# Performance work log

Hardware: AMD Instinct MI355X
Metric: run time of the kernel (lower is better)

The kernel has to match this reference:

```python
import jax, jax.numpy as jnp
import numpy as np

N = 512   # particles
T = 128   # timesteps
V_L = 3.4
V_0 = 4.2
GAMMA = 0.9
ALPHA = 0.15
BETA = 15.0
E_CRIT_INV = 2e-5
F_STD = 0.05
G_STD = 0.02
NU = 1.0 / (G_STD * float(np.sqrt(2.0 * np.pi)))
CUR_MIN = 0.0
CUR_MAX = 1.0


def voc(soc):
    # open-circuit voltage model
    return (V_L + (V_0 - V_L) * jnp.exp(GAMMA * (soc - 1.0))
            + ALPHA * V_L * (soc - 1.0)
            + (1.0 - ALPHA) * V_L * (jnp.exp(-BETA) - jnp.exp(-BETA * jnp.sqrt(soc))))


def mlp(x, w1, b1, w2, b2, w3, b3):
    h = jax.nn.sigmoid(x @ w1 + b1)
    h = jax.nn.sigmoid(h @ w2 + b2)
    return h @ w3 + b3


def setup_inputs() -> dict:
    key = jax.random.key(0)
    ks = jax.random.split(key, 11)
    soc_init = jax.random.uniform(ks[0], (N, 1), jnp.float32, 0.6, 1.0)
    current = jax.random.uniform(ks[1], (1, T), jnp.float32)
    voltage_measured = 3.4 + 0.8 * jax.random.uniform(ks[2], (1, T), jnp.float32)
    noise = jax.random.normal(ks[3], (T, N, 1), jnp.float32)
    u = jax.random.uniform(ks[4], (T,), jnp.float32)
    w1 = jax.random.normal(ks[5], (2, 1024), jnp.float32) / np.float32(np.sqrt(2.0))
    b1 = jnp.zeros((1024,), jnp.float32)
    w2 = jax.random.normal(ks[6], (1024, 512), jnp.float32) / np.float32(np.sqrt(1024.0))
    b2 = jnp.zeros((512,), jnp.float32)
    w3 = jax.random.normal(ks[7], (512, 1), jnp.float32) / np.float32(np.sqrt(512.0))
    b3 = jnp.zeros((1,), jnp.float32)
    return {"soc_init": soc_init, "current": current, "voltage_measured": voltage_measured,
            "noise": noise, "u": u, "w1": w1, "b1": b1, "w2": w2, "b2": b2, "w3": w3, "b3": b3}


def reference(soc_init, current, voltage_measured, noise, u, w1, b1, w2, b2, w3, b3):
    n = soc_init.shape[0]
    # pre-loop step: V at t=0 conditions
    I0 = current[0, 0] * jnp.ones_like(soc_init)
    sI0 = (I0 - CUR_MIN) / (CUR_MAX - CUR_MIN)
    Z0 = mlp(jnp.concatenate([soc_init, sI0], axis=1), w1, b1, w2, b2, w3, b3)
    V0 = voc(soc_init) - I0 * Z0

    log_n = jnp.log(jnp.float32(n))

    def step(carry, xs):
        soc, I, V = carry
        cur_t, vmeas_t, noise_t, u_t = xs
        # state propagation with process noise, then clamp to (0, 1]
        soc = soc - I * V * E_CRIT_INV + F_STD * noise_t
        soc = jnp.where(soc > 1.0, 1.0, jnp.where(soc < 0.0, 1e-10, soc))
        I = cur_t * jnp.ones_like(soc)
        sI = (I - CUR_MIN) / (CUR_MAX - CUR_MIN)
        Z = mlp(jnp.concatenate([soc, sI], axis=1), w1, b1, w2, b2, w3, b3)  # [N,1]
        V = voc(soc) - I * Z                                                 # [N,1]
        # importance weights / step loss (logsumexp trick as in source)
        logW = jnp.log(jnp.float32(NU)) - 0.5 * jnp.square((V - vmeas_t) / G_STD)
        step_loss = jax.nn.logsumexp(logW) - log_n
        # systematic resampling on normalized weights
        wn = jax.nn.softmax(logW[:, 0])          # normalized weights [N]
        cum = jnp.cumsum(wn)
        pos = (jnp.arange(n, dtype=jnp.float32) + u_t) / jnp.float32(n)
        idx = jnp.clip(jnp.searchsorted(cum, pos), 0, n - 1)
        soc_r = soc[idx]
        return (soc_r, I, V), (V[:, 0], soc_r[:, 0], step_loss)

    xs = (current[0], voltage_measured[0], noise, u)
    _, (v_hist, s_hist, losses) = jax.lax.scan(step, (soc_init, I0, V0), xs)
    loss = jnp.sum(losses)
    voltage = v_hist.T    # [N, T]
    soc_hist = s_hist.T   # [N, T]
    return loss, voltage, soc_hist
```

## Files before the change

kernel.cpp:

```cpp
#include <hip/hip_runtime.h>
#include <hip/hip_bf16.h>
#include <math.h>

#define N_PART 512
#define T_STEPS 128
#define G_NODES 33
#define TAB2D (G_NODES * G_NODES)
#define ROWS (T_STEPS * G_NODES)
#define V_L 3.4f
#define V_0 4.2f
#define GAMMA 0.9f
#define ALPHA 0.15f
#define BETA 15.0f
#define E_CRIT_INV 2e-5f
#define F_STD 0.05f
#define G_STD 0.02f

#define LBAR() asm volatile("s_waitcnt lgkmcnt(0)\n\ts_barrier" ::: "memory")

__device__ __forceinline__ float sigmoid_jax(float x) {
    float e = expf(-fabsf(x));
    float num = (x >= 0.f) ? 1.f : e;
    return num / (1.f + e);
}

__device__ __forceinline__ float vocf(float s) {
    float sm1 = s - 1.f;
    return V_L + (V_0 - V_L) * expf(GAMMA * sm1)
         + (ALPHA * V_L) * sm1
         + (1.f - ALPHA) * V_L * (expf(-BETA) - expf(-BETA * sqrtf(s)));
}

template <int R>
__device__ __forceinline__ int dpp_ror(int v) {
    return __builtin_amdgcn_update_dpp(0, v, 0x120 | R, 0xf, 0xf, false);
}
template <int S>
__device__ __forceinline__ int dpp_shr(int v) {
    return __builtin_amdgcn_update_dpp(0, v, 0x110 | S, 0xf, 0xf, true);
}
__device__ __forceinline__ float fror(float v, float o) { return o; }

__device__ __forceinline__ float wave_max_f(float v) {
    v = fmaxf(v, __int_as_float(dpp_ror<1>(__float_as_int(v))));
    v = fmaxf(v, __int_as_float(dpp_ror<2>(__float_as_int(v))));
    v = fmaxf(v, __int_as_float(dpp_ror<4>(__float_as_int(v))));
    v = fmaxf(v, __int_as_float(dpp_ror<8>(__float_as_int(v))));
    int iv = __float_as_int(v);
    v = fmaxf(v, __int_as_float(__builtin_amdgcn_update_dpp(iv, iv, 0x142, 0xf, 0xf, false)));
    iv = __float_as_int(v);
    v = fmaxf(v, __int_as_float(__builtin_amdgcn_update_dpp(iv, iv, 0x143, 0xf, 0xf, false)));
    return __int_as_float(__builtin_amdgcn_readlane(__float_as_int(v), 63));
}

__device__ __forceinline__ int wave_max_i(int v) {
    v = max(v, dpp_ror<1>(v));
    v = max(v, dpp_ror<2>(v));
    v = max(v, dpp_ror<4>(v));
    v = max(v, dpp_ror<8>(v));
    v = max(v, __builtin_amdgcn_update_dpp(v, v, 0x142, 0xf, 0xf, false));
    v = max(v, __builtin_amdgcn_update_dpp(v, v, 0x143, 0xf, 0xf, false));
    return __builtin_amdgcn_readlane(v, 63);
}

__device__ __forceinline__ float wave_scan_add(float v, int lane) {
    v += __int_as_float(dpp_shr<1>(__float_as_int(v)));
    v += __int_as_float(dpp_shr<2>(__float_as_int(v)));
    v += __int_as_float(dpp_shr<4>(__float_as_int(v)));
    v += __int_as_float(dpp_shr<8>(__float_as_int(v)));
    float s15 = __int_as_float(__builtin_amdgcn_readlane(__float_as_int(v), 15));
    float s31 = __int_as_float(__builtin_amdgcn_readlane(__float_as_int(v), 31));
    float s47 = __int_as_float(__builtin_amdgcn_readlane(__float_as_int(v), 47));
    int row = lane >> 4;
    if (row >= 1) v += s15;
    if (row >= 2) v += s31;
    if (row >= 3) v += s47;
    return v;
}

__device__ __forceinline__ int wave_scanmax_i(int v, int lane) {
    v = max(v, dpp_shr<1>(v));
    v = max(v, dpp_shr<2>(v));
    v = max(v, dpp_shr<4>(v));
    v = max(v, dpp_shr<8>(v));
    int r15 = __builtin_amdgcn_readlane(v, 15);
    int r31 = __builtin_amdgcn_readlane(v, 31);
    int r47 = __builtin_amdgcn_readlane(v, 47);
    int row = lane >> 4;
    if (row >= 1) v = max(v, r15);
    if (row >= 2) v = max(v, r31);
    if (row >= 3) v = max(v, r47);
    return v;
}

#define BKT 32
__global__ __launch_bounds__(256) void k_tab(
    const float* __restrict__ w1, const float* __restrict__ b1,
    const float* __restrict__ w2, const float* __restrict__ b2,
    const float* __restrict__ w3, float* __restrict__ zpart)
{
    const int tid = threadIdx.x;
    const int rowblk = blockIdx.x >> 1;
    const int colhalf = blockIdx.x & 1;
    const int r0 = rowblk * 8;
    const int cbase = colhalf * 256;

    __shared__ float As[8][BKT + 1];
    __shared__ float Bs[BKT][256];
    __shared__ float srow[8], irow[8];

    if (tid < 8) {
        int r = r0 + tid;
        r = r > (TAB2D - 1) ? (TAB2D - 1) : r;
        int si = r / G_NODES;
        int ii = r - si * G_NODES;
        srow[tid] = (float)si * (1.0f / 32.0f);
        irow[tid] = (float)ii * (1.0f / 32.0f);
    }
    __syncthreads();

    const int rg = tid >> 5;
    const int ct = tid & 31;
    float acc[8];
    #pragma unroll
    for (int b = 0; b < 8; ++b) acc[b] = 0.f;

    for (int kk = 0; kk < 1024; kk += BKT) {
        {
            int kc = kk + ct;
            float pre = srow[rg] * w1[kc] + irow[rg] * w1[1024 + kc] + b1[kc];
            As[rg][ct] = sigmoid_jax(pre);
        }
        #pragma unroll
        for (int jj = 0; jj < 8; ++jj) {
            int vi = tid + jj * 256;
            int k = vi >> 6, c4 = vi & 63;
            *(float4*)&Bs[k][c4 * 4] = *(const float4*)&w2[(kk + k) * 512 + cbase + c4 * 4];
        }
        __syncthreads();
        #pragma unroll
        for (int k = 0; k < BKT; ++k) {
            float a = As[rg][k];
            float bq[8];
            *(float4*)&bq[0] = *(const float4*)&Bs[k][ct * 4];
            *(float4*)&bq[4] = *(const float4*)&Bs[k][ct * 4 + 128];
            #pragma unroll
            for (int q = 0; q < 8; ++q) acc[q] += a * bq[q];
        }
        __syncthreads();
    }

    float b2r[8], w3r[8];
    *(float4*)&b2r[0] = *(const float4*)&b2[cbase + ct * 4];
    *(float4*)&b2r[4] = *(const float4*)&b2[cbase + ct * 4 + 128];
    *(float4*)&w3r[0] = *(const float4*)&w3[cbase + ct * 4];
    *(float4*)&w3r[4] = *(const float4*)&w3[cbase + ct * 4 + 128];
    float zp = 0.f;
    #pragma unroll
    for (int q = 0; q < 8; ++q)
        zp += w3r[q] * sigmoid_jax(acc[q] + b2r[q]);
    #pragma unroll
    for (int mm = 1; mm < 32; mm <<= 1) zp += __shfl_xor(zp, mm);
    if (ct == 0 && (r0 + rg) < TAB2D)
        zpart[colhalf * TAB2D + r0 + rg] = zp;
}

__device__ __forceinline__ float interp_tab(const float* __restrict__ row, int stride, float s) {
    float x = s * 32.0f;
    int j = (int)floorf(x);
    j = j < 0 ? 0 : (j > 31 ? 31 : j);
    int st = j - 1;
    st = st < 0 ? 0 : (st > 29 ? 29 : st);
    float uu = x - (float)st;
    float um0 = uu, um1 = uu - 1.f, um2 = uu - 2.f, um3 = uu - 3.f;
    float w0 = um1 * um2 * um3 * (-1.f / 6.f);
    float w1 = um0 * um2 * um3 * (0.5f);
    float w2 = um0 * um1 * um3 * (-0.5f);
    float w3 = um0 * um1 * um2 * (1.f / 6.f);
    return w0 * row[st * stride] + w1 * row[(st + 1) * stride]
         + w2 * row[(st + 2) * stride] + w3 * row[(st + 3) * stride];
}

__device__ __forceinline__ int count_le(float C, float u) {
    int h = (int)floorf(C - u);
    h = h < -1 ? -1 : (h > 511 ? 511 : h);
    h += (int)((h < 511) && (((float)(h + 1) + u) <= C));
    h += (int)((h < 511) && (((float)(h + 1) + u) <= C));
    h -= (int)((h >= 0) && (((float)h + u) > C));
    h -= (int)((h >= 0) && (((float)h + u) > C));
    return h + 1;
}

__global__ __launch_bounds__(512, 1) void k_seq(
    const float* __restrict__ zpart, const float* __restrict__ soc_init,
    const float* __restrict__ current, const float* __restrict__ vmeas,
    const float* __restrict__ u, const float* __restrict__ noise,
    const float* __restrict__ b3, float* __restrict__ vbuf,
    float* __restrict__ sbuf, float* __restrict__ out)
{
    const int tid = threadIdx.x;
    const int lane = tid & 63;
    const int wid = tid >> 6;

    __shared__ float zt[ROWS];
    __shared__ float zt2d[TAB2D];
    __shared__ float socs[2][512];
    __shared__ int marker[512];
    __shared__ float cur_s[128], vm_s[128], u_s[128];
    __shared__ float redM[8], redT[8];

    float bb3 = b3[0];
    for (int j = tid; j < TAB2D; j += 512) zt2d[j] = zpart[j] + zpart[TAB2D + j] + bb3;
    if (tid < 128) { cur_s[tid] = current[tid]; vm_s[tid] = vmeas[tid]; u_s[tid] = u[tid]; }
    marker[tid] = 0;
    __syncthreads();

    for (int idx = tid; idx < ROWS; idx += 512) {
        int t = idx / G_NODES;
        int g = idx - t * G_NODES;
        zt[idx] = interp_tab(&zt2d[g * G_NODES], 1, cur_s[t]);
    }
    __syncthreads();

    float soc = soc_init[tid];
    float Iprev = cur_s[0];
    float V = vocf(soc) - Iprev * interp_tab(&zt[0], 1, soc);
    float loss_acc = 0.f;
    const float LOG_NU = logf(19.947114020071635f);
    const float LOG_N = logf(512.f);

    float nz_cur = noise[tid];

    for (int t = 0; t < T_STEPS; ++t) {
        int tn = (t + 1 < T_STEPS) ? t + 1 : t;
        float nz_next = noise[tn * 512 + tid];

        soc = soc - Iprev * V * E_CRIT_INV + F_STD * nz_cur;
        soc = soc > 1.f ? 1.f : (soc < 0.f ? 1e-10f : soc);
        socs[t & 1][tid] = soc;

        float I = cur_s[t];
        V = vocf(soc) - I * interp_tab(&zt[t * G_NODES], 1, soc);
        float d = (V - vm_s[t]) * (1.f / G_STD);
        float lw = LOG_NU - 0.5f * d * d;

        float m = wave_max_f(lw);
        float e = expf(lw - m);
        float incl = wave_scan_add(e, lane);
        if (lane == 63) { redM[wid] = m; redT[wid] = incl; }
        LBAR();

        float rm = redM[lane & 7];
        float rt = redT[lane & 7];
        float M = rm;
        M = fmaxf(M, __int_as_float(dpp_ror<1>(__float_as_int(M))));
        M = fmaxf(M, __int_as_float(dpp_ror<2>(__float_as_int(M))));
        M = fmaxf(M, __int_as_float(dpp_ror<4>(__float_as_int(M))));
        M = fmaxf(M, __int_as_float(dpp_ror<8>(__float_as_int(M))));
        float fw = expf(rm - M);
        float term = rt * fw;
        float sc = term;
        sc += __int_as_float(dpp_shr<1>(__float_as_int(sc)));
        sc += __int_as_float(dpp_shr<2>(__float_as_int(sc)));
        sc += __int_as_float(dpp_shr<4>(__float_as_int(sc)));
        float S = __int_as_float(__builtin_amdgcn_readlane(__float_as_int(sc), 7));
        float off = 0.f;
        if (wid > 0) off = __int_as_float(__builtin_amdgcn_readlane(__float_as_int(sc), wid - 1));
        float fw_own = __int_as_float(__builtin_amdgcn_readlane(__float_as_int(fw), wid));
        loss_acc += M + logf(S) - LOG_N;

        float C = 512.f * ((off + incl * fw_own) / S);
        int hi = count_le(C, u_s[t]);
        if (hi < 512) atomicMax(&marker[hi], (t << 10) | (tid + 1));
        LBAR();

        int pm = 0;
        for (int w = 0; w < wid; ++w) pm = max(pm, marker[w * 64 + lane]);
        pm = wave_max_i(pm);
        int v = wave_scanmax_i(marker[tid], lane);
        int sv = max(v, pm);
        int owner = ((sv >> 10) == t) ? (sv & 1023) : 0;
        owner = owner > 511 ? 511 : owner;
        float socr = socs[t & 1][owner];

        vbuf[t * 512 + tid] = V;
        sbuf[t * 512 + tid] = socr;
        soc = socr;
        Iprev = I;
        nz_cur = nz_next;
    }
    if (tid == 0) out[0] = loss_acc;
}

__global__ __launch_bounds__(256) void k_fin(
    const float* __restrict__ vbuf, const float* __restrict__ sbuf,
    float* __restrict__ out)
{
    __shared__ float tile[32][33];
    int tz = blockIdx.z;
    int t0 = blockIdx.x * 32;
    int i0 = blockIdx.y * 32;
    const float* src = tz ? sbuf : vbuf;
    float* dst = out + 1 + tz * (N_PART * T_STEPS);
    int tx = threadIdx.x & 31, ty = threadIdx.x >> 5;
    #pragma unroll
    for (int m2 = 0; m2 < 4; ++m2)
        tile[ty + 8 * m2][tx] = src[(t0 + ty + 8 * m2) * 512 + i0 + tx];
    __syncthreads();
    #pragma unroll
    for (int m2 = 0; m2 < 4; ++m2)
        dst[(i0 + ty + 8 * m2) * 128 + t0 + tx] = tile[tx][ty + 8 * m2];
}

extern "C" void kernel_launch(void* const* d_in, const int* in_sizes, int n_in,
                              void* d_out, int out_size, void* d_ws, size_t ws_size,
                              hipStream_t stream)
{
    const float* soc_init = (const float*)d_in[0];
    const float* current  = (const float*)d_in[1];
    const float* vmeas    = (const float*)d_in[2];
    const float* noise    = (const float*)d_in[3];
    const float* u        = (const float*)d_in[4];
    const float* w1 = (const float*)d_in[5];
    const float* b1 = (const float*)d_in[6];
    const float* w2 = (const float*)d_in[7];
    const float* b2 = (const float*)d_in[8];
    const float* w3 = (const float*)d_in[9];
    const float* b3 = (const float*)d_in[10];
    float* out = (float*)d_out;
    float* ws  = (float*)d_ws;

    float* zpart = ws;
    float* vbuf  = ws + 2 * TAB2D;
    float* sbuf  = vbuf + N_PART * T_STEPS;

    k_tab<<<274, 256, 0, stream>>>(w1, b1, w2, b2, w3, zpart);
    k_seq<<<1, 512, 0, stream>>>(zpart, soc_init, current, vmeas, u, noise, b3,
                                 vbuf, sbuf, out);
    k_fin<<<dim3(4, 16, 2), 256, 0, stream>>>(vbuf, sbuf, out);
}
```

Baseline: 286.2 us.

## Replace marker-based resampling with direct range scatter and retile table GEMM

The resampling step now has each particle compute its lower and upper cumulative-count bounds and write its SOC into the resampled slots it owns. This replaces the atomicMax marker array and the prefix-max scans that followed it. The cross-wave combine now uses readlane broadcasts instead of DPP scans, and exp/log switch to the fast intrinsics. The table-building kernel handles 16 rows per block with one column per thread, halving the block count. These changes shorten the serial per-timestep critical path, at the cost of a per-thread loop that can be uneven and slightly lower-precision exp/log.

```diff
diff --git a/kernel.cpp b/kernel.cpp
--- a/kernel.cpp
+++ b/kernel.cpp
@@ -1,20 +1,19 @@
 #include <hip/hip_runtime.h>
-#include <hip/hip_bf16.h>
 #include <math.h>
 
-#define N_PART 512
-#define T_STEPS 128
-#define G_NODES 33
-#define TAB2D (G_NODES * G_NODES)
-#define ROWS (T_STEPS * G_NODES)
-#define V_L 3.4f
-#define V_0 4.2f
-#define GAMMA 0.9f
-#define ALPHA 0.15f
-#define BETA 15.0f
-#define E_CRIT_INV 2e-5f
-#define F_STD 0.05f
-#define G_STD 0.02f
+#define NP 512
+#define TS 128
+#define GI 33
+#define TAB2D (GI * GI)
+#define ROWS (TS * GI)
+#define V_Lc 3.4f
+#define V_0c 4.2f
+#define GAMMAc 0.9f
+#define ALPHAc 0.15f
+#define BETAc 15.0f
+#define E_INV 2e-5f
+#define F_STDc 0.05f
+#define G_STDc 0.02f
 
 #define LBAR() asm volatile("s_waitcnt lgkmcnt(0)\n\ts_barrier" ::: "memory")
 
@@ -26,9 +25,9 @@
 
 __device__ __forceinline__ float vocf(float s) {
     float sm1 = s - 1.f;
-    return V_L + (V_0 - V_L) * expf(GAMMA * sm1)
-         + (ALPHA * V_L) * sm1
-         + (1.f - ALPHA) * V_L * (expf(-BETA) - expf(-BETA * sqrtf(s)));
+    return V_Lc + (V_0c - V_Lc) * expf(GAMMAc * sm1)
+         + (ALPHAc * V_Lc) * sm1
+         + (1.f - ALPHAc) * V_Lc * (expf(-BETAc) - expf(-BETAc * sqrtf(s)));
 }
 
 template <int R>
@@ -39,7 +38,9 @@
 __device__ __forceinline__ int dpp_shr(int v) {
     return __builtin_amdgcn_update_dpp(0, v, 0x110 | S, 0xf, 0xf, true);
 }
-__device__ __forceinline__ float fror(float v, float o) { return o; }
+__device__ __forceinline__ float rdlane_f(float v, int l) {
+    return __int_as_float(__builtin_amdgcn_readlane(__float_as_int(v), l));
+}
 
 __device__ __forceinline__ float wave_max_f(float v) {
     v = fmaxf(v, __int_as_float(dpp_ror<1>(__float_as_int(v))));
@@ -50,17 +51,7 @@
     v = fmaxf(v, __int_as_float(__builtin_amdgcn_update_dpp(iv, iv, 0x142, 0xf, 0xf, false)));
     iv = __float_as_int(v);
     v = fmaxf(v, __int_as_float(__builtin_amdgcn_update_dpp(iv, iv, 0x143, 0xf, 0xf, false)));
-    return __int_as_float(__builtin_amdgcn_readlane(__float_as_int(v), 63));
-}
-
-__device__ __forceinline__ int wave_max_i(int v) {
-    v = max(v, dpp_ror<1>(v));
-    v = max(v, dpp_ror<2>(v));
-    v = max(v, dpp_ror<4>(v));
-    v = max(v, dpp_ror<8>(v));
-    v = max(v, __builtin_amdgcn_update_dpp(v, v, 0x142, 0xf, 0xf, false));
-    v = max(v, __builtin_amdgcn_update_dpp(v, v, 0x143, 0xf, 0xf, false));
-    return __builtin_amdgcn_readlane(v, 63);
+    return rdlane_f(v, 63);
 }
 
 __device__ __forceinline__ float wave_scan_add(float v, int lane) {
@@ -68,9 +59,9 @@
     v += __int_as_float(dpp_shr<2>(__float_as_int(v)));
     v += __int_as_float(dpp_shr<4>(__float_as_int(v)));
     v += __int_as_float(dpp_shr<8>(__float_as_int(v)));
-    float s15 = __int_as_float(__builtin_amdgcn_readlane(__float_as_int(v), 15));
-    float s31 = __int_as_float(__builtin_amdgcn_readlane(__float_as_int(v), 31));
-    float s47 = __int_as_float(__builtin_amdgcn_readlane(__float_as_int(v), 47));
+    float s15 = rdlane_f(v, 15);
+    float s31 = rdlane_f(v, 31);
+    float s47 = rdlane_f(v, 47);
     int row = lane >> 4;
     if (row >= 1) v += s15;
     if (row >= 2) v += s31;
@@ -78,58 +69,80 @@
     return v;
 }
 
-__device__ __forceinline__ int wave_scanmax_i(int v, int lane) {
-    v = max(v, dpp_shr<1>(v));
-    v = max(v, dpp_shr<2>(v));
-    v = max(v, dpp_shr<4>(v));
-    v = max(v, dpp_shr<8>(v));
-    int r15 = __builtin_amdgcn_readlane(v, 15);
-    int r31 = __builtin_amdgcn_readlane(v, 31);
-    int r47 = __builtin_amdgcn_readlane(v, 47);
-    int row = lane >> 4;
-    if (row >= 1) v = max(v, r15);
-    if (row >= 2) v = max(v, r31);
-    if (row >= 3) v = max(v, r47);
-    return v;
-}
-
-#define BKT 32
+__device__ __forceinline__ float shfl_up1_f(float v, int lane, float lane0val) {
+    float pv = __int_as_float(dpp_shr<1>(__float_as_int(v)));
+    float r15 = rdlane_f(v, 15);
+    float r31 = rdlane_f(v, 31);
+    float r47 = rdlane_f(v, 47);
+    if (lane == 16) pv = r15;
+    if (lane == 32) pv = r31;
+    if (lane == 48) pv = r47;
+    if (lane == 0)  pv = lane0val;
+    return pv;
+}
+
+__device__ __forceinline__ float interp_z(const float* __restrict__ row, float s) {
+    float x = s * 32.0f;
+    int j = (int)floorf(x);
+    j = j < 0 ? 0 : (j > 31 ? 31 : j);
+    int st = j - 1;
+    st = st < 0 ? 0 : (st > 29 ? 29 : st);
+    float uu = x - (float)st;
+    float um0 = uu, um1 = uu - 1.f, um2 = uu - 2.f, um3 = uu - 3.f;
+    float c0 = um1 * um2 * um3 * (-1.f / 6.f);
+    float c1 = um0 * um2 * um3 * (0.5f);
+    float c2 = um0 * um1 * um3 * (-0.5f);
+    float c3 = um0 * um1 * um2 * (1.f / 6.f);
+    return c0 * row[st] + c1 * row[st + 1] + c2 * row[st + 2] + c3 * row[st + 3];
+}
+
+__device__ __forceinline__ int count_le(float C, float u) {
+    int h = (int)floorf(C - u);
+    h = h < -1 ? -1 : (h > 511 ? 511 : h);
+    h += (int)((h < 511) && (((float)(h + 1) + u) <= C));
+    h += (int)((h < 511) && (((float)(h + 1) + u) <= C));
+    h -= (int)((h >= 0) && (((float)h + u) > C));
+    h -= (int)((h >= 0) && (((float)h + u) > C));
+    return h + 1;
+}
+
 __global__ __launch_bounds__(256) void k_tab(
     const float* __restrict__ w1, const float* __restrict__ b1,
     const float* __restrict__ w2, const float* __restrict__ b2,
     const float* __restrict__ w3, float* __restrict__ zpart)
 {
     const int tid = threadIdx.x;
+    const int lane = tid & 63;
+    const int wv = tid >> 6;
     const int rowblk = blockIdx.x >> 1;
     const int colhalf = blockIdx.x & 1;
-    const int r0 = rowblk * 8;
+    const int r0 = rowblk * 16;
     const int cbase = colhalf * 256;
 
-    __shared__ float As[8][BKT + 1];
-    __shared__ float Bs[BKT][256];
-    __shared__ float srow[8], irow[8];
-
-    if (tid < 8) {
-        int r = r0 + tid;
-        r = r > (TAB2D - 1) ? (TAB2D - 1) : r;
-        int si = r / G_NODES;
-        int ii = r - si * G_NODES;
+    __shared__ float As[16][33];
+    __shared__ float Bs[32][256];
+    __shared__ float srow[16], irow[16];
+    __shared__ float red[16][4];
+
+    if (tid < 16) {
+        int r = r0 + tid; if (r > TAB2D - 1) r = TAB2D - 1;
+        int si = r / GI, ii = r - si * GI;
         srow[tid] = (float)si * (1.0f / 32.0f);
         irow[tid] = (float)ii * (1.0f / 32.0f);
     }
     __syncthreads();
 
-    const int rg = tid >> 5;
-    const int ct = tid & 31;
-    float acc[8];
+    float acc[16];
     #pragma unroll
-    for (int b = 0; b < 8; ++b) acc[b] = 0.f;
-
-    for (int kk = 0; kk < 1024; kk += BKT) {
-        {
-            int kc = kk + ct;
-            float pre = srow[rg] * w1[kc] + irow[rg] * w1[1024 + kc] + b1[kc];
-            As[rg][ct] = sigmoid_jax(pre);
+    for (int r = 0; r < 16; ++r) acc[r] = 0.f;
+
+    for (int kk = 0; kk < 1024; kk += 32) {
+        #pragma unroll
+        for (int h = 0; h < 2; ++h) {
+            int idx = tid + h * 256;
+            int row = idx >> 5, k = idx & 31, kc = kk + k;
+            float pre = srow[row] * w1[kc] + irow[row] * w1[1024 + kc] + b1[kc];
+            As[row][k] = sigmoid_jax(pre);
         }
         #pragma unroll
         for (int jj = 0; jj < 8; ++jj) {
@@ -139,56 +152,28 @@
         }
         __syncthreads();
         #pragma unroll
-        for (int k = 0; k < BKT; ++k) {
-            float a = As[rg][k];
-            float bq[8];
-            *(float4*)&bq[0] = *(const float4*)&Bs[k][ct * 4];
-            *(float4*)&bq[4] = *(const float4*)&Bs[k][ct * 4 + 128];
+        for (int k = 0; k < 32; ++k) {
+            float bv = Bs[k][tid];
             #pragma unroll
-            for (int q = 0; q < 8; ++q) acc[q] += a * bq[q];
+            for (int r = 0; r < 16; ++r) acc[r] += As[r][k] * bv;
         }
         __syncthreads();
     }
 
-    float b2r[8], w3r[8];
-    *(float4*)&b2r[0] = *(const float4*)&b2[cbase + ct * 4];
-    *(float4*)&b2r[4] = *(const float4*)&b2[cbase + ct * 4 + 128];
-    *(float4*)&w3r[0] = *(const float4*)&w3[cbase + ct * 4];
-    *(float4*)&w3r[4] = *(const float4*)&w3[cbase + ct * 4 + 128];
-    float zp = 0.f;
+    float b2c = b2[cbase + tid];
+    float w3c = w3[cbase + tid];
     #pragma unroll
-    for (int q = 0; q < 8; ++q)
-        zp += w3r[q] * sigmoid_jax(acc[q] + b2r[q]);
-    #pragma unroll
-    for (int mm = 1; mm < 32; mm <<= 1) zp += __shfl_xor(zp, mm);
-    if (ct == 0 && (r0 + rg) < TAB2D)
-        zpart[colhalf * TAB2D + r0 + rg] = zp;
-}
-
-__device__ __forceinline__ float interp_tab(const float* __restrict__ row, int stride, float s) {
-    float x = s * 32.0f;
-    int j = (int)floorf(x);
-    j = j < 0 ? 0 : (j > 31 ? 31 : j);
-    int st = j - 1;
-    st = st < 0 ? 0 : (st > 29 ? 29 : st);
-    float uu = x - (float)st;
-    float um0 = uu, um1 = uu - 1.f, um2 = uu - 2.f, um3 = uu - 3.f;
-    float w0 = um1 * um2 * um3 * (-1.f / 6.f);
-    float w1 = um0 * um2 * um3 * (0.5f);
-    float w2 = um0 * um1 * um3 * (-0.5f);
-    float w3 = um0 * um1 * um2 * (1.f / 6.f);
-    return w0 * row[st * stride] + w1 * row[(st + 1) * stride]
-         + w2 * row[(st + 2) * stride] + w3 * row[(st + 3) * stride];
-}
-
-__device__ __forceinline__ int count_le(float C, float u) {
-    int h = (int)floorf(C - u);
-    h = h < -1 ? -1 : (h > 511 ? 511 : h);
-    h += (int)((h < 511) && (((float)(h + 1) + u) <= C));
-    h += (int)((h < 511) && (((float)(h + 1) + u) <= C));
-    h -= (int)((h >= 0) && (((float)h + u) > C));
-    h -= (int)((h >= 0) && (((float)h + u) > C));
-    return h + 1;
+    for (int r = 0; r < 16; ++r) {
+        float zp = w3c * sigmoid_jax(acc[r] + b2c);
+        #pragma unroll
+        for (int mm = 1; mm < 64; mm <<= 1) zp += __shfl_xor(zp, mm);
+        if (lane == 0) red[r][wv] = zp;
+    }
+    __syncthreads();
+    if (tid < 16 && (r0 + tid) < TAB2D) {
+        float s = ((red[tid][0] + red[tid][1]) + red[tid][2]) + red[tid][3];
+        zpart[colhalf * TAB2D + r0 + tid] = s;
+    }
 }
 
 __global__ __launch_bounds__(512, 1) void k_seq(
@@ -200,90 +185,81 @@
 {
     const int tid = threadIdx.x;
     const int lane = tid & 63;
-    const int wid = tid >> 6;
-
-    __shared__ float zt[ROWS];
+    const int wv = tid >> 6;
+    const int swv = __builtin_amdgcn_readfirstlane(wv);
+
+    __shared__ float zt[TS][GI];
     __shared__ float zt2d[TAB2D];
-    __shared__ float socs[2][512];
-    __shared__ int marker[512];
-    __shared__ float cur_s[128], vm_s[128], u_s[128];
+    __shared__ float socs_r[2][NP];
+    __shared__ float cur_s[TS], vm_s[TS], u_s[TS];
     __shared__ float redM[8], redT[8];
 
     float bb3 = b3[0];
     for (int j = tid; j < TAB2D; j += 512) zt2d[j] = zpart[j] + zpart[TAB2D + j] + bb3;
-    if (tid < 128) { cur_s[tid] = current[tid]; vm_s[tid] = vmeas[tid]; u_s[tid] = u[tid]; }
-    marker[tid] = 0;
-    __syncthreads();
-
+    if (tid < TS) { cur_s[tid] = current[tid]; vm_s[tid] = vmeas[tid]; u_s[tid] = u[tid]; }
+    __syncthreads();
     for (int idx = tid; idx < ROWS; idx += 512) {
-        int t = idx / G_NODES;
-        int g = idx - t * G_NODES;
-        zt[idx] = interp_tab(&zt2d[g * G_NODES], 1, cur_s[t]);
+        int t = idx / GI, g = idx - t * GI;
+        zt[t][g] = interp_z(&zt2d[g * GI], cur_s[t]);
     }
     __syncthreads();
 
     float soc = soc_init[tid];
     float Iprev = cur_s[0];
-    float V = vocf(soc) - Iprev * interp_tab(&zt[0], 1, soc);
+    float V = vocf(soc) - Iprev * interp_z(&zt[0][0], soc);
     float loss_acc = 0.f;
     const float LOG_NU = logf(19.947114020071635f);
     const float LOG_N = logf(512.f);
-
     float nz_cur = noise[tid];
 
-    for (int t = 0; t < T_STEPS; ++t) {
-        int tn = (t + 1 < T_STEPS) ? t + 1 : t;
+    for (int t = 0; t < TS; ++t) {
+        int tn = (t + 1 < TS) ? t + 1 : t;
         float nz_next = noise[tn * 512 + tid];
 
-        soc = soc - Iprev * V * E_CRIT_INV + F_STD * nz_cur;
+        soc = soc - Iprev * V * E_INV + F_STDc * nz_cur;
         soc = soc > 1.f ? 1.f : (soc < 0.f ? 1e-10f : soc);
-        socs[t & 1][tid] = soc;
 
         float I = cur_s[t];
-        V = vocf(soc) - I * interp_tab(&zt[t * G_NODES], 1, soc);
-        float d = (V - vm_s[t]) * (1.f / G_STD);
+        V = vocf(soc) - I * interp_z(&zt[t][0], soc);
+        float d = (V - vm_s[t]) * (1.f / G_STDc);
         float lw = LOG_NU - 0.5f * d * d;
 
         float m = wave_max_f(lw);
-        float e = expf(lw - m);
+        float e = __expf(lw - m);
         float incl = wave_scan_add(e, lane);
-        if (lane == 63) { redM[wid] = m; redT[wid] = incl; }
+        if (lane == 63) { redM[wv] = m; redT[wv] = incl; }
         LBAR();
 
         float rm = redM[lane & 7];
         float rt = redT[lane & 7];
-        float M = rm;
-        M = fmaxf(M, __int_as_float(dpp_ror<1>(__float_as_int(M))));
-        M = fmaxf(M, __int_as_float(dpp_ror<2>(__float_as_int(M))));
-        M = fmaxf(M, __int_as_float(dpp_ror<4>(__float_as_int(M))));
-        M = fmaxf(M, __int_as_float(dpp_ror<8>(__float_as_int(M))));
-        float fw = expf(rm - M);
-        float term = rt * fw;
-        float sc = term;
-        sc += __int_as_float(dpp_shr<1>(__float_as_int(sc)));
-        sc += __int_as_float(dpp_shr<2>(__float_as_int(sc)));
-        sc += __int_as_float(dpp_shr<4>(__float_as_int(sc)));
-        float S = __int_as_float(__builtin_amdgcn_readlane(__float_as_int(sc), 7));
+        float m0 = rdlane_f(rm, 0), m1 = rdlane_f(rm, 1), m2 = rdlane_f(rm, 2), m3 = rdlane_f(rm, 3);
+        float m4 = rdlane_f(rm, 4), m5 = rdlane_f(rm, 5), m6 = rdlane_f(rm, 6), m7 = rdlane_f(rm, 7);
+        float M = fmaxf(fmaxf(fmaxf(m0, m1), fmaxf(m2, m3)),
+                        fmaxf(fmaxf(m4, m5), fmaxf(m6, m7)));
+        float fw = __expf(rm - M);
+        float tt = rt * fw;
+        float t0 = rdlane_f(tt, 0), t1 = rdlane_f(tt, 1), t2 = rdlane_f(tt, 2), t3 = rdlane_f(tt, 3);
+        float t4 = rdlane_f(tt, 4), t5 = rdlane_f(tt, 5), t6 = rdlane_f(tt, 6), t7 = rdlane_f(tt, 7);
+        float p1 = t0 + t1, p2 = p1 + t2, p3 = p2 + t3, p4 = p3 + t4, p5 = p4 + t5, p6 = p5 + t6;
+        float S = p6 + t7;
         float off = 0.f;
-        if (wid > 0) off = __int_as_float(__builtin_amdgcn_readlane(__float_as_int(sc), wid - 1));
-        float fw_own = __int_as_float(__builtin_amdgcn_readlane(__float_as_int(fw), wid));
-        loss_acc += M + logf(S) - LOG_N;
+        off = (swv > 0) ? ((swv == 1) ? t0 : (swv == 2) ? p1 : (swv == 3) ? p2 :
+                           (swv == 4) ? p3 : (swv == 5) ? p4 : (swv == 6) ? p5 : p6) : 0.f;
+        float fw_own = rdlane_f(fw, swv);
+        loss_acc += M + __logf(S) - LOG_N;
 
         float C = 512.f * ((off + incl * fw_own) / S);
-        int hi = count_le(C, u_s[t]);
-        if (hi < 512) atomicMax(&marker[hi], (t << 10) | (tid + 1));
+        float C0 = 512.f * (off / S);
+        float pC = shfl_up1_f(C, lane, C0);
+        float ut = u_s[t];
+        int hi = count_le(C, ut);
+        int lo = count_le(pC, ut);
+
+        for (int s2 = lo; s2 < hi; ++s2) socs_r[t & 1][s2] = soc;
+        vbuf[t * 512 + tid] = V;
         LBAR();
 
-        int pm = 0;
-        for (int w = 0; w < wid; ++w) pm = max(pm, marker[w * 64 + lane]);
-        pm = wave_max_i(pm);
-        int v = wave_scanmax_i(marker[tid], lane);
-        int sv = max(v, pm);
-        int owner = ((sv >> 10) == t) ? (sv & 1023) : 0;
-        owner = owner > 511 ? 511 : owner;
-        float socr = socs[t & 1][owner];
-
-        vbuf[t * 512 + tid] = V;
+        float socr = socs_r[t & 1][tid];
         sbuf[t * 512 + tid] = socr;
         soc = socr;
         Iprev = I;
@@ -301,7 +277,7 @@
     int t0 = blockIdx.x * 32;
     int i0 = blockIdx.y * 32;
     const float* src = tz ? sbuf : vbuf;
-    float* dst = out + 1 + tz * (N_PART * T_STEPS);
+    float* dst = out + 1 + tz * (NP * TS);
     int tx = threadIdx.x & 31, ty = threadIdx.x >> 5;
     #pragma unroll
     for (int m2 = 0; m2 < 4; ++m2)
@@ -331,10 +307,10 @@
     float* ws  = (float*)d_ws;
 
     float* zpart = ws;
-    float* vbuf  = ws + 2 * TAB2D;
-    float* sbuf  = vbuf + N_PART * T_STEPS;
-
-    k_tab<<<274, 256, 0, stream>>>(w1, b1, w2, b2, w3, zpart);
+    float* vbuf  = ws + 2 * TAB2D + 2;
+    float* sbuf  = vbuf + NP * TS;
+
+    k_tab<<<138, 256, 0, stream>>>(w1, b1, w2, b2, w3, zpart);
     k_seq<<<1, 512, 0, stream>>>(zpart, soc_init, current, vmeas, u, noise, b3,
                                  vbuf, sbuf, out);
     k_fin<<<dim3(4, 16, 2), 256, 0, stream>>>(vbuf, sbuf, out);
```

New measurement: 559.0 us. 95.3% more time.
